# Performance work log

Measured on AMD Instinct MI355X. Metric: run time of the kernel, lower is better.

## Reference

```python
import jax, jax.numpy as jnp
import numpy as np

N = 50000      # nodes
E = 800000     # edges
H = 4          # attention heads
C = 64         # per-head channels (channel_in = channel_out = 64)
DIN = 128      # raw node feature dim (lazy Linear infers this)
D1 = H * C     # 256 = channel_in*4 concat dim
EPS = 1e-16    # PyG softmax eps
LN_EPS = 1e-5


def setup_inputs() -> dict:
    key = jax.random.key(0)
    ks = jax.random.split(key, 20)
    p = lambda k, shape: jax.random.normal(k, shape, jnp.float32) * 0.05
    return {
        "x": jax.random.normal(ks[0], (N, DIN), jnp.float32),
        "edge_index": jax.random.randint(ks[1], (2, E), 0, N, jnp.int32),
        # conv1 (GATConv with separate src/dst transforms, bipartite lazy mode)
        "Wsrc1": p(ks[2], (DIN, D1)), "Wdst1": p(ks[3], (DIN, D1)),
        "atts1": p(ks[4], (H, C)), "attd1": p(ks[5], (H, C)), "b1": p(ks[6], (D1,)),
        # lin1 skip
        "Wlin1": p(ks[7], (DIN, D1)), "blin1": p(ks[8], (D1,)),
        # LayerNorm
        "gamma": jnp.ones((D1,), jnp.float32), "beta": jnp.zeros((D1,), jnp.float32),
        # conv2
        "Wsrc2": p(ks[9], (D1, D1)), "Wdst2": p(ks[10], (D1, D1)),
        "atts2": p(ks[11], (H, C)), "attd2": p(ks[12], (H, C)), "b2": p(ks[13], (D1,)),
        # lin2 skip
        "Wlin2": p(ks[14], (D1, D1)), "blin2": p(ks[15], (D1,)),
    }


def gat_conv(x, src, dst, Wsrc, Wdst, atts, attd, bias):
    """PyG GATConv: gather -> leaky_relu score -> segment softmax over dst -> scatter-add."""
    n = x.shape[0]
    xs = (x @ Wsrc).reshape(n, H, C)   # source-side transform
    xd = (x @ Wdst).reshape(n, H, C)   # destination-side transform
    a_s = jnp.sum(xs * atts, axis=-1)  # [N,H]
    a_d = jnp.sum(xd * attd, axis=-1)  # [N,H]
    e = jax.nn.leaky_relu(a_s[src] + a_d[dst], 0.2)          # [E,H]
    m = jax.ops.segment_max(e, dst, num_segments=n)           # [N,H]
    m = jnp.where(jnp.isfinite(m), m, 0.0)                    # nodes with no in-edges
    ex = jnp.exp(e - m[dst])
    den = jax.ops.segment_sum(ex, dst, num_segments=n)
    alpha = ex / (den[dst] + EPS)                             # [E,H]
    out = jax.ops.segment_sum(xs[src] * alpha[:, :, None], dst, num_segments=n)
    return out.reshape(n, H * C) + bias                       # concat heads + bias


def reference(x, edge_index, Wsrc1, Wdst1, atts1, attd1, b1, Wlin1, blin1,
              gamma, beta, Wsrc2, Wdst2, atts2, attd2, b2, Wlin2, blin2):
    src, dst = edge_index[0], edge_index[1]
    h = gat_conv(x, src, dst, Wsrc1, Wdst1, atts1, attd1, b1) + x @ Wlin1 + blin1
    mu = jnp.mean(h, axis=-1, keepdims=True)
    var = jnp.mean((h - mu) ** 2, axis=-1, keepdims=True)
    h = (h - mu) * jax.lax.rsqrt(var + LN_EPS) * gamma + beta
    h = jax.nn.relu(h)
    out = gat_conv(h, src, dst, Wsrc2, Wdst2, atts2, attd2, b2) + h @ Wlin2 + blin2
    return out
```

## Files before the change

kernel.cpp:

```cpp
#include <hip/hip_runtime.h>
#include <float.h>

constexpr int DIN = 128;
constexpr int D1  = 256;
constexpr int HH  = 4;
constexpr int CC  = 64;

typedef _Float16 f16;
typedef __attribute__((ext_vector_type(2))) _Float16 f16x2;
typedef __attribute__((ext_vector_type(4))) _Float16 f16x4;
typedef __attribute__((ext_vector_type(8))) _Float16 f16x8;
typedef __attribute__((ext_vector_type(4))) float f32x4;

#if __has_builtin(__builtin_amdgcn_fdot2)
#define HAS_FDOT2 1
#else
#define HAS_FDOT2 0
#endif

__device__ __forceinline__ float wave_sum(float v) {
    #pragma unroll
    for (int off = 32; off > 0; off >>= 1) v += __shfl_down(v, off, 64);
    return v;
}

__global__ __launch_bounds__(256) void pack_w_all_kernel(
        const float* __restrict__ Wsrc1, const float* __restrict__ Wlin1,
        const float* __restrict__ Wsrc2, const float* __restrict__ Wlin2,
        f16* __restrict__ WpS1, f16* __restrict__ WpL1,
        f16* __restrict__ WpS2, f16* __restrict__ WpL2) {
    int idx = blockIdx.x * 256 + threadIdx.x;
    const float *Wa, *Wb;
    f16 *Wpa, *Wpb;
    if (idx < DIN * D1) { Wa = Wsrc1; Wb = Wlin1; Wpa = WpS1; Wpb = WpL1; }
    else {
        idx -= DIN * D1;
        if (idx >= D1 * D1) return;
        Wa = Wsrc2; Wb = Wlin2; Wpa = WpS2; Wpb = WpL2;
    }
    int j    = idx & 7;
    int lane = (idx >> 3) & 63;
    int t    = idx >> 9;
    int ct   = t & 15, kt = t >> 4;
    int k    = kt * 32 + (lane >> 4) * 8 + j;
    int col  = ct * 16 + (lane & 15);
    size_t widx = (size_t)k * D1 + col;
    Wpa[idx] = (f16)Wa[widx];
    Wpb[idx] = (f16)Wb[widx];
}

__global__ __launch_bounds__(512) void make_v_all_kernel(
        const float* __restrict__ Wsrc1, const float* __restrict__ Wdst1,
        const float* __restrict__ atts1, const float* __restrict__ attd1,
        const float* __restrict__ Wsrc2, const float* __restrict__ Wdst2,
        const float* __restrict__ atts2, const float* __restrict__ attd2,
        float* __restrict__ Vs1, float* __restrict__ Vd1,
        float* __restrict__ Vs2, float* __restrict__ Vd2) {
    int kb = blockIdx.x;
    int w = threadIdx.x >> 6, lane = threadIdx.x & 63;
    int mat = w >> 2, h = w & 3;
    const float *W, *att;
    float* V;
    int k;
    if (kb < DIN) {
        k = kb;
        W = mat ? Wdst1 : Wsrc1; att = mat ? attd1 : atts1; V = mat ? Vd1 : Vs1;
    } else {
        k = kb - DIN;
        W = mat ? Wdst2 : Wsrc2; att = mat ? attd2 : atts2; V = mat ? Vd2 : Vs2;
    }
    float v = W[(size_t)k * D1 + h * CC + lane] * att[h * CC + lane];
    v = wave_sum(v);
    if (lane == 0) V[k * HH + h] = v;
}

__global__ __launch_bounds__(256) void cvt_scores_kernel(
        const float* __restrict__ X, const float* __restrict__ Vs,
        const float* __restrict__ Vd, f16* __restrict__ X16,
        float* __restrict__ a_s, float* __restrict__ a_d, int n) {
    constexpr int K = DIN, C = 32, SH = 5;
    __shared__ float4 VsL[K + 4];
    __shared__ float4 VdL[K + 4];
    for (int k = threadIdx.x; k < K; k += 256) {
        int ki = k + (k >> SH);
        VsL[ki] = reinterpret_cast<const float4*>(Vs)[k];
        VdL[ki] = reinterpret_cast<const float4*>(Vd)[k];
    }
    __syncthreads();

    const int lane  = threadIdx.x & 63;
    const int wid   = threadIdx.x >> 6;
    const int node  = blockIdx.x * 64 + wid * 16 + (lane >> 2);
    const int chunk = lane & 3;
    const int nodec = min(node, n - 1);
    const float* xp = X + (size_t)nodec * K + chunk * C;

    float xv[C];
    #pragma unroll
    for (int b = 0; b < C / 4; ++b) {
        float4 v = reinterpret_cast<const float4*>(xp)[b];
        xv[b * 4 + 0] = v.x; xv[b * 4 + 1] = v.y;
        xv[b * 4 + 2] = v.z; xv[b * 4 + 3] = v.w;
    }
    if (node < n) {
        f16* op = X16 + (size_t)node * K + chunk * C;
        #pragma unroll
        for (int b = 0; b < C / 8; ++b) {
            f16x8 o;
            #pragma unroll
            for (int t = 0; t < 8; ++t) o[t] = (f16)xv[b * 8 + t];
            reinterpret_cast<f16x8*>(op)[b] = o;
        }
    }

    float ps0 = 0.f, ps1 = 0.f, ps2 = 0.f, ps3 = 0.f;
    float pd0 = 0.f, pd1 = 0.f, pd2 = 0.f, pd3 = 0.f;
    #pragma unroll
    for (int t = 0; t < C; ++t) {
        int k  = chunk * C + t;
        int ki = k + (k >> SH);
        float xf = xv[t];
        float4 vs = VsL[ki];
        float4 vd = VdL[ki];
        ps0 = fmaf(xf, vs.x, ps0); ps1 = fmaf(xf, vs.y, ps1);
        ps2 = fmaf(xf, vs.z, ps2); ps3 = fmaf(xf, vs.w, ps3);
        pd0 = fmaf(xf, vd.x, pd0); pd1 = fmaf(xf, vd.y, pd1);
        pd2 = fmaf(xf, vd.z, pd2); pd3 = fmaf(xf, vd.w, pd3);
    }
    #pragma unroll
    for (int off = 1; off <= 2; off <<= 1) {
        ps0 += __shfl_xor(ps0, off, 64); ps1 += __shfl_xor(ps1, off, 64);
        ps2 += __shfl_xor(ps2, off, 64); ps3 += __shfl_xor(ps3, off, 64);
        pd0 += __shfl_xor(pd0, off, 64); pd1 += __shfl_xor(pd1, off, 64);
        pd2 += __shfl_xor(pd2, off, 64); pd3 += __shfl_xor(pd3, off, 64);
    }
    if (node < n) {
        float psv = chunk == 0 ? ps0 : chunk == 1 ? ps1 : chunk == 2 ? ps2 : ps3;
        float pdv = chunk == 0 ? pd0 : chunk == 1 ? pd1 : chunk == 2 ? pd2 : pd3;
        a_s[node * 4 + chunk] = psv;
        a_d[node * 4 + chunk] = pdv;
    }
}

__global__ __launch_bounds__(256) void deg_kernel(
        const int* __restrict__ dst, int* __restrict__ deg, int ne) {
    int e = blockIdx.x * 256 + threadIdx.x;
    if (e < ne) atomicAdd(deg + dst[e], 1);
}

__global__ __launch_bounds__(1024) void scan_phase1(
        const int* __restrict__ deg, int* __restrict__ partial,
        int* __restrict__ blocksum, int n) {
    __shared__ int tmp[1024];
    const int tid = threadIdx.x;
    int i = blockIdx.x * 1024 + tid;
    int v = (i < n) ? deg[i] : 0;
    tmp[tid] = v;
    __syncthreads();
    #pragma unroll
    for (int off = 1; off < 1024; off <<= 1) {
        int t = (tid >= off) ? tmp[tid - off] : 0;
        __syncthreads();
        tmp[tid] += t;
        __syncthreads();
    }
    if (i < n) partial[i] = tmp[tid];
    if (tid == 1023) blocksum[blockIdx.x] = tmp[1023];
}

__global__ __launch_bounds__(64) void scan_phase2(int* __restrict__ bs, int nb) {
    int lane = threadIdx.x;
    if (nb <= 64) {
        int v = (lane < nb) ? bs[lane] : 0;
        #pragma unroll
        for (int off = 1; off < 64; off <<= 1) {
            int t = __shfl_up(v, off, 64);
            if (lane >= off) v += t;
        }
        if (lane < nb) bs[lane] = v;
    } else if (lane == 0) {
        int acc = 0;
        for (int i = 0; i < nb; ++i) { acc += bs[i]; bs[i] = acc; }
    }
}

__global__ __launch_bounds__(1024) void scan_phase3(
        const int* __restrict__ partial, const int* __restrict__ bs,
        const int* __restrict__ deg, int* __restrict__ rowptr,
        int* __restrict__ degcur, int n) {
    int i = blockIdx.x * 1024 + threadIdx.x;
    if (i >= n) return;
    int add  = blockIdx.x ? bs[blockIdx.x - 1] : 0;
    int incl = partial[i] + add;
    rowptr[i + 1] = incl;
    degcur[i] = incl - deg[i];
    if (i == 0) rowptr[0] = 0;
}

__global__ __launch_bounds__(256) void fill_kernel(
        const int* __restrict__ src, const int* __restrict__ dst,
        int* __restrict__ cursor, int* __restrict__ srcs_csr, int ne) {
    int e = blockIdx.x * 256 + threadIdx.x;
    if (e >= ne) return;
    int pos = atomicAdd(cursor + dst[e], 1);
    srcs_csr[pos] = src[e];
}

template <int K, typename TO2>
__global__ __launch_bounds__(256) void gemm_dual_mfma(
        const f16* __restrict__ A, const f16* __restrict__ Wp1,
        const f16* __restrict__ Wp2, const float* __restrict__ bias1,
        const float* __restrict__ bias2, f16* __restrict__ O1,
        TO2* __restrict__ O2, int n) {
    constexpr int KT = K / 32;
    const int lane = threadIdx.x & 63;
    const int w    = threadIdx.x >> 6;
    const int row0 = blockIdx.x * 64;
    const int col0 = w * 64;

    f32x4 acc1[4][4], acc2[4][4];
    const f32x4 zero = {0.f, 0.f, 0.f, 0.f};
    #pragma unroll
    for (int i = 0; i < 4; ++i)
        #pragma unroll
        for (int j = 0; j < 4; ++j) { acc1[i][j] = zero; acc2[i][j] = zero; }

    const f16* Arow[4];
    #pragma unroll
    for (int rf = 0; rf < 4; ++rf) {
        int ar = min(row0 + rf * 16 + (lane & 15), n - 1);
        Arow[rf] = A + (size_t)ar * K + (lane >> 4) * 8;
    }
    const f16* Wb1 = Wp1 + ((size_t)(w * 4) * 64 + lane) * 8;
    const f16* Wb2 = Wp2 + ((size_t)(w * 4) * 64 + lane) * 8;

    #pragma unroll
    for (int kt = 0; kt < KT; ++kt) {
        f16x8 a[4];
        #pragma unroll
        for (int rf = 0; rf < 4; ++rf)
            a[rf] = *reinterpret_cast<const f16x8*>(Arow[rf] + kt * 32);
        #pragma unroll
        for (int cf = 0; cf < 4; ++cf) {
            f16x8 b1v = *reinterpret_cast<const f16x8*>(Wb1 + (size_t)(kt * 16 + cf) * 512);
            f16x8 b2v = *reinterpret_cast<const f16x8*>(Wb2 + (size_t)(kt * 16 + cf) * 512);
            #pragma unroll
            for (int rf = 0; rf < 4; ++rf) {
                acc1[rf][cf] = __builtin_amdgcn_mfma_f32_16x16x32_f16(a[rf], b1v, acc1[rf][cf], 0, 0, 0);
                acc2[rf][cf] = __builtin_amdgcn_mfma_f32_16x16x32_f16(a[rf], b2v, acc2[rf][cf], 0, 0, 0);
            }
        }
    }

    #pragma unroll
    for (int cf = 0; cf < 4; ++cf) {
        const int col = col0 + cf * 16 + (lane & 15);
        const float bsum = bias1[col] + bias2[col];
        #pragma unroll
        for (int rf = 0; rf < 4; ++rf) {
            #pragma unroll
            for (int r = 0; r < 4; ++r) {
                const int row = row0 + rf * 16 + (lane >> 4) * 4 + r;
                if (row < n) {
                    O1[(size_t)row * D1 + col] = (f16)acc1[rf][cf][r];
                    O2[(size_t)row * D1 + col] = (TO2)(acc2[rf][cf][r] + bsum);
                }
            }
        }
    }
}

__device__ __forceinline__ float sel4(float4 v, int h) {
    return h == 0 ? v.x : h == 1 ? v.y : h == 2 ? v.z : v.w;
}
__device__ __forceinline__ float4 lrelu4(float4 as, float4 ad) {
    float4 e;
    e.x = as.x + ad.x; e.x = e.x > 0.f ? e.x : 0.2f * e.x;
    e.y = as.y + ad.y; e.y = e.y > 0.f ? e.y : 0.2f * e.y;
    e.z = as.z + ad.z; e.z = e.z > 0.f ? e.z : 0.2f * e.z;
    e.w = as.w + ad.w; e.w = e.w > 0.f ? e.w : 0.2f * e.w;
    return e;
}

#define ALDS_STRIDE 66

__device__ __forceinline__ float4 gat_node_acc(
        const int* __restrict__ srcs, const float* __restrict__ a_s,
        const f16* __restrict__ xs, f16* __restrict__ alds,
        float4 ad4, int base, int deg, int lane) {
    const int h = lane >> 4;
    float4 den = {0.f, 0.f, 0.f, 0.f};
    float4 acc = {0.f, 0.f, 0.f, 0.f};
    const f16* arow = alds + h * ALDS_STRIDE;

    for (int c0 = 0; c0 < deg; c0 += 64) {
        const int cnt = min(64, deg - c0);
        const int idx = c0 + lane;
        const bool valid = idx < deg;
        const int sl = srcs[base + min(idx, deg - 1)];
        {
            float4 as = *reinterpret_cast<const float4*>(a_s + (size_t)sl * 4);
            float4 e = lrelu4(as, ad4);
            float a0 = valid ? __expf(e.x) : 0.f;
            float a1 = valid ? __expf(e.y) : 0.f;
            float a2 = valid ? __expf(e.z) : 0.f;
            float a3 = valid ? __expf(e.w) : 0.f;
            den.x += a0; den.y += a1; den.z += a2; den.w += a3;
            alds[0 * ALDS_STRIDE + lane] = (f16)a0;
            alds[1 * ALDS_STRIDE + lane] = (f16)a1;
            alds[2 * ALDS_STRIDE + lane] = (f16)a2;
            alds[3 * ALDS_STRIDE + lane] = (f16)a3;
        }
        asm volatile("s_waitcnt lgkmcnt(0)" ::: "memory");

        const int sv = sl;
        for (int i = 0; i < cnt; i += 4) {
            int s1 = __shfl(sv, i, 64);
            int s2 = __shfl(sv, i + 1, 64);
            int s3 = __shfl(sv, i + 2, 64);
            int s4 = __shfl(sv, i + 3, 64);
            f16x2 alA = *reinterpret_cast<const f16x2*>(arow + i);
            f16x2 alB = *reinterpret_cast<const f16x2*>(arow + i + 2);
            uint2 x1 = *reinterpret_cast<const uint2*>(xs + (size_t)s1 * D1 + lane * 4);
            uint2 x2 = *reinterpret_cast<const uint2*>(xs + (size_t)s2 * D1 + lane * 4);
            uint2 x3 = *reinterpret_cast<const uint2*>(xs + (size_t)s3 * D1 + lane * 4);
            uint2 x4 = *reinterpret_cast<const uint2*>(xs + (size_t)s4 * D1 + lane * 4);
#if HAS_FDOT2
            unsigned pA0 = __builtin_amdgcn_perm(x1.x, x2.x, 0x01000504u);
            unsigned pA1 = __builtin_amdgcn_perm(x1.x, x2.x, 0x03020706u);
            unsigned pA2 = __builtin_amdgcn_perm(x1.y, x2.y, 0x01000504u);
            unsigned pA3 = __builtin_amdgcn_perm(x1.y, x2.y, 0x03020706u);
            acc.x = __builtin_amdgcn_fdot2(__builtin_bit_cast(f16x2, pA0), alA, acc.x, false);
            acc.y = __builtin_amdgcn_fdot2(__builtin_bit_cast(f16x2, pA1), alA, acc.y, false);
            acc.z = __builtin_amdgcn_fdot2(__builtin_bit_cast(f16x2, pA2), alA, acc.z, false);
            acc.w = __builtin_amdgcn_fdot2(__builtin_bit_cast(f16x2, pA3), alA, acc.w, false);
            unsigned pB0 = __builtin_amdgcn_perm(x3.x, x4.x, 0x01000504u);
            unsigned pB1 = __builtin_amdgcn_perm(x3.x, x4.x, 0x03020706u);
            unsigned pB2 = __builtin_amdgcn_perm(x3.y, x4.y, 0x01000504u);
            unsigned pB3 = __builtin_amdgcn_perm(x3.y, x4.y, 0x03020706u);
            acc.x = __builtin_amdgcn_fdot2(__builtin_bit_cast(f16x2, pB0), alB, acc.x, false);
            acc.y = __builtin_amdgcn_fdot2(__builtin_bit_cast(f16x2, pB1), alB, acc.y, false);
            acc.z = __builtin_amdgcn_fdot2(__builtin_bit_cast(f16x2, pB2), alB, acc.z, false);
            acc.w = __builtin_amdgcn_fdot2(__builtin_bit_cast(f16x2, pB3), alB, acc.w, false);
#else
            f16x4 a1v = __builtin_bit_cast(f16x4, x1);
            f16x4 a2v = __builtin_bit_cast(f16x4, x2);
            f16x4 a3v = __builtin_bit_cast(f16x4, x3);
            f16x4 a4v = __builtin_bit_cast(f16x4, x4);
            float w1 = (float)alA.x, w2 = (float)alA.y;
            float w3 = (float)alB.x, w4 = (float)alB.y;
            acc.x = fmaf((float)a1v[0], w1, acc.x); acc.x = fmaf((float)a2v[0], w2, acc.x);
            acc.y = fmaf((float)a1v[1], w1, acc.y); acc.y = fmaf((float)a2v[1], w2, acc.y);
            acc.z = fmaf((float)a1v[2], w1, acc.z); acc.z = fmaf((float)a2v[2], w2, acc.z);
            acc.w = fmaf((float)a1v[3], w1, acc.w); acc.w = fmaf((float)a4v[3], w2, acc.w);
            acc.x = fmaf((float)a3v[0], w3, acc.x); acc.x = fmaf((float)a4v[0], w4, acc.x);
            acc.y = fmaf((float)a3v[1], w3, acc.y); acc.y = fmaf((float)a4v[1], w4, acc.y);
            acc.z = fmaf((float)a3v[2], w3, acc.z); acc.z = fmaf((float)a4v[2], w4, acc.z);
            acc.w = fmaf((float)a3v[3], w3, acc.w); acc.w = fmaf((float)a4v[3], w4, acc.w);
#endif
        }
    }

    #pragma unroll
    for (int off = 1; off < 64; off <<= 1) {
        den.x += __shfl_xor(den.x, off, 64);
        den.y += __shfl_xor(den.y, off, 64);
        den.z += __shfl_xor(den.z, off, 64);
        den.w += __shfl_xor(den.w, off, 64);
    }
    const float invd = 1.f / (sel4(den, h) + 1e-16f);
    acc.x *= invd; acc.y *= invd; acc.z *= invd; acc.w *= invd;
    return acc;
}

__global__ __launch_bounds__(256) void gat_gather_ln_kernel(
        const int* __restrict__ rowptr, const int* __restrict__ srcs,
        const float* __restrict__ a_s1, const float* __restrict__ a_d1,
        const f16* __restrict__ xs, const f16* __restrict__ skip,
        const float* __restrict__ gamma, const float* __restrict__ beta,
        const float* __restrict__ Vs2, const float* __restrict__ Vd2,
        f16* __restrict__ hout, float* __restrict__ a_s2,
        float* __restrict__ a_d2, int n) {
    __shared__ f16 alpha_lds[4][4 * ALDS_STRIDE];
    const int wid = threadIdx.x >> 6, lane = threadIdx.x & 63;
    const int d = blockIdx.x * 4 + wid;
    if (d >= n) return;
    const int base = rowptr[d];
    const int deg  = rowptr[d + 1] - base;

    float4 acc = {0.f, 0.f, 0.f, 0.f};
    if (deg > 0) {
        const float4 ad4 = *reinterpret_cast<const float4*>(a_d1 + (size_t)d * 4);
        acc = gat_node_acc(srcs, a_s1, xs, alpha_lds[wid], ad4, base, deg, lane);
    }

    f16x4 sk = *reinterpret_cast<const f16x4*>(skip + (size_t)d * D1 + lane * 4);
    float4 v;
    v.x = acc.x + (float)sk[0];
    v.y = acc.y + (float)sk[1];
    v.z = acc.z + (float)sk[2];
    v.w = acc.w + (float)sk[3];

    float s  = v.x + v.y + v.z + v.w;
    float sq = v.x * v.x + v.y * v.y + v.z * v.z + v.w * v.w;
    #pragma unroll
    for (int off = 32; off > 0; off >>= 1) {
        s  += __shfl_down(s, off, 64);
        sq += __shfl_down(sq, off, 64);
    }
    s  = __shfl(s, 0, 64);
    sq = __shfl(sq, 0, 64);
    float mu  = s * (1.f / 256.f);
    float var = sq * (1.f / 256.f) - mu * mu;
    float rstd = rsqrtf(var + 1e-5f);
    float4 g = *reinterpret_cast<const float4*>(gamma + lane * 4);
    float4 b = *reinterpret_cast<const float4*>(beta + lane * 4);
    f16x4 o;
    o[0] = (f16)fmaxf((v.x - mu) * rstd * g.x + b.x, 0.f);
    o[1] = (f16)fmaxf((v.y - mu) * rstd * g.y + b.y, 0.f);
    o[2] = (f16)fmaxf((v.z - mu) * rstd * g.z + b.z, 0.f);
    o[3] = (f16)fmaxf((v.w - mu) * rstd * g.w + b.w, 0.f);
    *reinterpret_cast<f16x4*>(hout + (size_t)d * D1 + lane * 4) = o;

    float of0 = (float)o[0], of1 = (float)o[1], of2 = (float)o[2], of3 = (float)o[3];
    const float4* V4s = reinterpret_cast<const float4*>(Vs2);
    const float4* V4d = reinterpret_cast<const float4*>(Vd2);
    float4 r0 = V4s[lane * 4 + 0], r1 = V4s[lane * 4 + 1];
    float4 r2 = V4s[lane * 4 + 2], r3 = V4s[lane * 4 + 3];
    float4 ps;
    ps.x = of0 * r0.x + of1 * r1.x + of2 * r2.x + of3 * r3.x;
    ps.y = of0 * r0.y + of1 * r1.y + of2 * r2.y + of3 * r3.y;
    ps.z = of0 * r0.z + of1 * r1.z + of2 * r2.z + of3 * r3.z;
    ps.w = of0 * r0.w + of1 * r1.w + of2 * r2.w + of3 * r3.w;
    r0 = V4d[lane * 4 + 0]; r1 = V4d[lane * 4 + 1];
    r2 = V4d[lane * 4 + 2]; r3 = V4d[lane * 4 + 3];
    float4 pd;
    pd.x = of0 * r0.x + of1 * r1.x + of2 * r2.x + of3 * r3.x;
    pd.y = of0 * r0.y + of1 * r1.y + of2 * r2.y + of3 * r3.y;
    pd.z = of0 * r0.z + of1 * r1.z + of2 * r2.z + of3 * r3.z;
    pd.w = of0 * r0.w + of1 * r1.w + of2 * r2.w + of3 * r3.w;
    #pragma unroll
    for (int off = 1; off < 64; off <<= 1) {
        ps.x += __shfl_xor(ps.x, off, 64); ps.y += __shfl_xor(ps.y, off, 64);
        ps.z += __shfl_xor(ps.z, off, 64); ps.w += __shfl_xor(ps.w, off, 64);
        pd.x += __shfl_xor(pd.x, off, 64); pd.y += __shfl_xor(pd.y, off, 64);
        pd.z += __shfl_xor(pd.z, off, 64); pd.w += __shfl_xor(pd.w, off, 64);
    }
    if (lane == 0) {
        *reinterpret_cast<float4*>(a_s2 + (size_t)d * 4) = ps;
        *reinterpret_cast<float4*>(a_d2 + (size_t)d * 4) = pd;
    }
}

__global__ __launch_bounds__(256) void gat_gather_out_kernel(
        const int* __restrict__ rowptr, const int* __restrict__ srcs,
        const float* __restrict__ a_s, const float* __restrict__ a_d,
        const f16* __restrict__ xs, float* __restrict__ out, int n) {
    __shared__ f16 alpha_lds[4][4 * ALDS_STRIDE];
    const int wid = threadIdx.x >> 6, lane = threadIdx.x & 63;
    const int d = blockIdx.x * 4 + wid;
    if (d >= n) return;
    const int base = rowptr[d];
    const int deg  = rowptr[d + 1] - base;
    if (deg == 0) return;
    const float4 ad4 = *reinterpret_cast<const float4*>(a_d + (size_t)d * 4);
    float4 acc = gat_node_acc(srcs, a_s, xs, alpha_lds[wid], ad4, base, deg, lane);
    float* o = out + (size_t)d * D1 + lane * 4;
    float4 ov = *reinterpret_cast<const float4*>(o);
    ov.x += acc.x; ov.y += acc.y; ov.z += acc.z; ov.w += acc.w;
    *reinterpret_cast<float4*>(o) = ov;
}

extern "C" void kernel_launch(void* const* d_in, const int* in_sizes, int n_in,
                              void* d_out, int out_size, void* d_ws, size_t ws_size,
                              hipStream_t stream) {
    const float* x     = (const float*)d_in[0];
    const int*   ei    = (const int*)d_in[1];
    const float* Wsrc1 = (const float*)d_in[2];
    const float* Wdst1 = (const float*)d_in[3];
    const float* atts1 = (const float*)d_in[4];
    const float* attd1 = (const float*)d_in[5];
    const float* b1    = (const float*)d_in[6];
    const float* Wlin1 = (const float*)d_in[7];
    const float* blin1 = (const float*)d_in[8];
    const float* gamma = (const float*)d_in[9];
    const float* beta  = (const float*)d_in[10];
    const float* Wsrc2 = (const float*)d_in[11];
    const float* Wdst2 = (const float*)d_in[12];
    const float* atts2 = (const float*)d_in[13];
    const float* attd2 = (const float*)d_in[14];
    const float* b2    = (const float*)d_in[15];
    const float* Wlin2 = (const float*)d_in[16];
    const float* blin2 = (const float*)d_in[17];

    const int n  = in_sizes[0] / DIN;
    const int ne = in_sizes[1] / 2;
    const int* src = ei;
    const int* dst = ei + ne;

    char* w8 = (char*)d_ws;
    size_t off = 0;
    auto alloc = [&](size_t bytes) -> void* {
        void* p = w8 + off;
        off += (bytes + 255) & ~(size_t)255;
        return p;
    };
    f16*  h16    = (f16*)alloc((size_t)n * D1 * 2);
    f16*  x16    = h16;
    f16*  xs16   = (f16*)alloc((size_t)n * D1 * 2);
    f16*  skip1  = (f16*)alloc((size_t)n * D1 * 2);
    float* a_s1  = (float*)alloc((size_t)n * HH * 4);
    float* a_d1  = (float*)alloc((size_t)n * HH * 4);
    float* a_s2  = (float*)alloc((size_t)n * HH * 4);
    float* a_d2  = (float*)alloc((size_t)n * HH * 4);
    float* Vs1   = (float*)alloc((size_t)D1 * HH * 4);
    float* Vd1   = (float*)alloc((size_t)D1 * HH * 4);
    float* Vs2   = (float*)alloc((size_t)D1 * HH * 4);
    float* Vd2   = (float*)alloc((size_t)D1 * HH * 4);
    int* rowptr   = (int*)alloc(((size_t)n + 1) * 4);
    int* degbuf   = (int*)alloc((size_t)n * 4);
    int* degcur   = (int*)alloc((size_t)n * 4);
    int* partial  = (int*)alloc((size_t)n * 4);
    int* blocksum = (int*)alloc(1024 * 4);
    int* srcs_csr = (int*)alloc((size_t)ne * 4);
    f16* WpS1  = (f16*)alloc((size_t)DIN * D1 * 2);
    f16* WpL1  = (f16*)alloc((size_t)DIN * D1 * 2);
    f16* WpS2  = (f16*)alloc((size_t)D1 * D1 * 2);
    f16* WpL2  = (f16*)alloc((size_t)D1 * D1 * 2);

    float* out = (float*)d_out;

    const int nb_node4  = (n + 3) / 4;
    const int nb_node64 = (n + 63) / 64;
    const int nb_e      = (ne + 255) / 256;
    const int nb_gemm   = (n + 63) / 64;
    const int nb_scan   = (n + 1023) / 1024;
    const int nb_pack   = (DIN * D1 + D1 * D1 + 255) / 256;

    hipMemsetAsync(degbuf, 0, (size_t)n * 4, stream);
    deg_kernel<<<nb_e, 256, 0, stream>>>(dst, degbuf, ne);
    scan_phase1<<<nb_scan, 1024, 0, stream>>>(degbuf, partial, blocksum, n);
    scan_phase2<<<1, 64, 0, stream>>>(blocksum, nb_scan);
    scan_phase3<<<nb_scan, 1024, 0, stream>>>(partial, blocksum, degbuf, rowptr, degcur, n);
    fill_kernel<<<nb_e, 256, 0, stream>>>(src, dst, degcur, srcs_csr, ne);
    pack_w_all_kernel<<<nb_pack, 256, 0, stream>>>(Wsrc1, Wlin1, Wsrc2, Wlin2,
                                                   WpS1, WpL1, WpS2, WpL2);
    make_v_all_kernel<<<DIN + D1, 512, 0, stream>>>(Wsrc1, Wdst1, atts1, attd1,
                                                    Wsrc2, Wdst2, atts2, attd2,
                                                    Vs1, Vd1, Vs2, Vd2);

    cvt_scores_kernel<<<nb_node64, 256, 0, stream>>>(x, Vs1, Vd1, x16, a_s1, a_d1, n);
    gemm_dual_mfma<DIN, f16><<<nb_gemm, 256, 0, stream>>>(x16, WpS1, WpL1, b1, blin1, xs16, skip1, n);
    gat_gather_ln_kernel<<<nb_node4, 256, 0, stream>>>(rowptr, srcs_csr, a_s1, a_d1, xs16,
                                                       skip1, gamma, beta, Vs2, Vd2,
                                                       h16, a_s2, a_d2, n);

    gemm_dual_mfma<D1, float><<<nb_gemm, 256, 0, stream>>>(h16, WpS2, WpL2, b2, blin2, xs16, out, n);
    gat_gather_out_kernel<<<nb_node4, 256, 0, stream>>>(rowptr, srcs_csr, a_s2, a_d2, xs16, out, n);
}
```

Measured before the change: 330.0 us.

## Split GAT aggregation into alpha precompute and column-sliced gather kernels

Attention coefficients are now computed and normalized once per edge into a head-major f16 buffer by a separate kernel. The aggregation is then split across 8 column slices per node, with 8 lanes per node. Blocks with the same slice index touch the same narrow column band of xs, which is meant to improve cache locality of the random gathers. LayerNorm and the second-layer skip add become separate passes over an intermediate buffer. The cost is extra launches and extra global traffic for the alpha and gather buffers, plus f16 rounding of the normalized alphas.

```diff
diff --git a/kernel.cpp b/kernel.cpp
--- a/kernel.cpp
+++ b/kernel.cpp
@@ -206,12 +206,12 @@
     srcs_csr[pos] = src[e];
 }
 
-template <int K, typename TO2>
+template <int K>
 __global__ __launch_bounds__(256) void gemm_dual_mfma(
         const f16* __restrict__ A, const f16* __restrict__ Wp1,
         const f16* __restrict__ Wp2, const float* __restrict__ bias1,
         const float* __restrict__ bias2, f16* __restrict__ O1,
-        TO2* __restrict__ O2, int n) {
+        f16* __restrict__ O2, int n) {
     constexpr int KT = K / 32;
     const int lane = threadIdx.x & 63;
     const int w    = threadIdx.x >> 6;
@@ -263,16 +263,13 @@
                 const int row = row0 + rf * 16 + (lane >> 4) * 4 + r;
                 if (row < n) {
                     O1[(size_t)row * D1 + col] = (f16)acc1[rf][cf][r];
-                    O2[(size_t)row * D1 + col] = (TO2)(acc2[rf][cf][r] + bsum);
+                    O2[(size_t)row * D1 + col] = (f16)(acc2[rf][cf][r] + bsum);
                 }
             }
         }
     }
 }
 
-__device__ __forceinline__ float sel4(float4 v, int h) {
-    return h == 0 ? v.x : h == 1 ? v.y : h == 2 ? v.z : v.w;
-}
 __device__ __forceinline__ float4 lrelu4(float4 as, float4 ad) {
     float4 e;
     e.x = as.x + ad.x; e.x = e.x > 0.f ? e.x : 0.2f * e.x;
@@ -282,23 +279,49 @@
     return e;
 }
 
-#define ALDS_STRIDE 66
-
-__device__ __forceinline__ float4 gat_node_acc(
-        const int* __restrict__ srcs, const float* __restrict__ a_s,
-        const f16* __restrict__ xs, f16* __restrict__ alds,
-        float4 ad4, int base, int deg, int lane) {
-    const int h = lane >> 4;
-    float4 den = {0.f, 0.f, 0.f, 0.f};
-    float4 acc = {0.f, 0.f, 0.f, 0.f};
-    const f16* arow = alds + h * ALDS_STRIDE;
-
-    for (int c0 = 0; c0 < deg; c0 += 64) {
-        const int cnt = min(64, deg - c0);
-        const int idx = c0 + lane;
-        const bool valid = idx < deg;
-        const int sl = srcs[base + min(idx, deg - 1)];
-        {
+__global__ __launch_bounds__(256) void alpha16_kernel(
+        const int* __restrict__ rowptr, const int* __restrict__ srcs,
+        const float* __restrict__ a_s, const float* __restrict__ a_d,
+        f16* __restrict__ alphaT, int ne, int n) {
+    const int lane = threadIdx.x & 63;
+    const int wid  = threadIdx.x >> 6;
+    const int g    = lane & 15;
+    const int d    = blockIdx.x * 16 + wid * 4 + (lane >> 4);
+    if (d >= n) return;
+    const int base = rowptr[d];
+    const int deg  = rowptr[d + 1] - base;
+    if (deg == 0) return;
+    const float4 ad4 = *reinterpret_cast<const float4*>(a_d + (size_t)d * 4);
+
+    if (deg <= 16) {
+        const bool valid = g < deg;
+        const int sl = srcs[base + min(g, deg - 1)];
+        float4 as = *reinterpret_cast<const float4*>(a_s + (size_t)sl * 4);
+        float4 e = lrelu4(as, ad4);
+        float a0 = valid ? __expf(e.x) : 0.f;
+        float a1 = valid ? __expf(e.y) : 0.f;
+        float a2 = valid ? __expf(e.z) : 0.f;
+        float a3 = valid ? __expf(e.w) : 0.f;
+        float4 den = {a0, a1, a2, a3};
+        #pragma unroll
+        for (int off = 1; off < 16; off <<= 1) {
+            den.x += __shfl_xor(den.x, off, 16);
+            den.y += __shfl_xor(den.y, off, 16);
+            den.z += __shfl_xor(den.z, off, 16);
+            den.w += __shfl_xor(den.w, off, 16);
+        }
+        if (valid) {
+            alphaT[0 * (size_t)ne + base + g] = (f16)(a0 / (den.x + 1e-16f));
+            alphaT[1 * (size_t)ne + base + g] = (f16)(a1 / (den.y + 1e-16f));
+            alphaT[2 * (size_t)ne + base + g] = (f16)(a2 / (den.z + 1e-16f));
+            alphaT[3 * (size_t)ne + base + g] = (f16)(a3 / (den.w + 1e-16f));
+        }
+    } else {
+        float4 den = {0.f, 0.f, 0.f, 0.f};
+        for (int c0 = 0; c0 < deg; c0 += 16) {
+            int idx = c0 + g;
+            bool valid = idx < deg;
+            int sl = srcs[base + min(idx, deg - 1)];
             float4 as = *reinterpret_cast<const float4*>(a_s + (size_t)sl * 4);
             float4 e = lrelu4(as, ad4);
             float a0 = valid ? __expf(e.x) : 0.f;
@@ -306,100 +329,142 @@
             float a2 = valid ? __expf(e.z) : 0.f;
             float a3 = valid ? __expf(e.w) : 0.f;
             den.x += a0; den.y += a1; den.z += a2; den.w += a3;
-            alds[0 * ALDS_STRIDE + lane] = (f16)a0;
-            alds[1 * ALDS_STRIDE + lane] = (f16)a1;
-            alds[2 * ALDS_STRIDE + lane] = (f16)a2;
-            alds[3 * ALDS_STRIDE + lane] = (f16)a3;
-        }
-        asm volatile("s_waitcnt lgkmcnt(0)" ::: "memory");
-
-        const int sv = sl;
-        for (int i = 0; i < cnt; i += 4) {
-            int s1 = __shfl(sv, i, 64);
-            int s2 = __shfl(sv, i + 1, 64);
-            int s3 = __shfl(sv, i + 2, 64);
-            int s4 = __shfl(sv, i + 3, 64);
-            f16x2 alA = *reinterpret_cast<const f16x2*>(arow + i);
-            f16x2 alB = *reinterpret_cast<const f16x2*>(arow + i + 2);
-            uint2 x1 = *reinterpret_cast<const uint2*>(xs + (size_t)s1 * D1 + lane * 4);
-            uint2 x2 = *reinterpret_cast<const uint2*>(xs + (size_t)s2 * D1 + lane * 4);
-            uint2 x3 = *reinterpret_cast<const uint2*>(xs + (size_t)s3 * D1 + lane * 4);
-            uint2 x4 = *reinterpret_cast<const uint2*>(xs + (size_t)s4 * D1 + lane * 4);
+            if (valid) {
+                alphaT[0 * (size_t)ne + base + idx] = (f16)a0;
+                alphaT[1 * (size_t)ne + base + idx] = (f16)a1;
+                alphaT[2 * (size_t)ne + base + idx] = (f16)a2;
+                alphaT[3 * (size_t)ne + base + idx] = (f16)a3;
+            }
+        }
+        #pragma unroll
+        for (int off = 1; off < 16; off <<= 1) {
+            den.x += __shfl_xor(den.x, off, 16);
+            den.y += __shfl_xor(den.y, off, 16);
+            den.z += __shfl_xor(den.z, off, 16);
+            den.w += __shfl_xor(den.w, off, 16);
+        }
+        float i0 = 1.f / (den.x + 1e-16f);
+        float i1 = 1.f / (den.y + 1e-16f);
+        float i2 = 1.f / (den.z + 1e-16f);
+        float i3 = 1.f / (den.w + 1e-16f);
+        for (int idx = g; idx < deg; idx += 16) {
+            alphaT[0 * (size_t)ne + base + idx] = (f16)((float)alphaT[0 * (size_t)ne + base + idx] * i0);
+            alphaT[1 * (size_t)ne + base + idx] = (f16)((float)alphaT[1 * (size_t)ne + base + idx] * i1);
+            alphaT[2 * (size_t)ne + base + idx] = (f16)((float)alphaT[2 * (size_t)ne + base + idx] * i2);
+            alphaT[3 * (size_t)ne + base + idx] = (f16)((float)alphaT[3 * (size_t)ne + base + idx] * i3);
+        }
+    }
+}
+
+__device__ __forceinline__ float4 gather_slice_acc(
+        const int* __restrict__ srcs, const f16* __restrict__ ap,
+        const f16* __restrict__ xs, int base, int deg, int coloff, int g) {
+    float4 acc = {0.f, 0.f, 0.f, 0.f};
+    for (int c0 = 0; c0 < deg; c0 += 8) {
+        const int idx = c0 + g;
+        const int sl = __builtin_nontemporal_load(srcs + base + min(idx, deg - 1));
+        int abit = 0;
+        if (idx < deg)
+            abit = (int)__builtin_nontemporal_load(
+                reinterpret_cast<const unsigned short*>(ap + base + idx));
+        const int cnt = min(8, deg - c0);
+        for (int i = 0; i < cnt; i += 2) {
+            int s1 = __shfl(sl, i, 8);
+            int s2 = __shfl(sl, i + 1, 8);
+            int a1 = __shfl(abit, i, 8);
+            int a2 = __shfl(abit, i + 1, 8);
+            unsigned au = (unsigned)(a1 & 0xffff) | ((unsigned)a2 << 16);
+            f16x2 al2 = __builtin_bit_cast(f16x2, au);
+            uint2 x1 = *reinterpret_cast<const uint2*>(xs + (size_t)s1 * D1 + coloff);
+            uint2 x2 = *reinterpret_cast<const uint2*>(xs + (size_t)s2 * D1 + coloff);
 #if HAS_FDOT2
-            unsigned pA0 = __builtin_amdgcn_perm(x1.x, x2.x, 0x01000504u);
-            unsigned pA1 = __builtin_amdgcn_perm(x1.x, x2.x, 0x03020706u);
-            unsigned pA2 = __builtin_amdgcn_perm(x1.y, x2.y, 0x01000504u);
-            unsigned pA3 = __builtin_amdgcn_perm(x1.y, x2.y, 0x03020706u);
-            acc.x = __builtin_amdgcn_fdot2(__builtin_bit_cast(f16x2, pA0), alA, acc.x, false);
-            acc.y = __builtin_amdgcn_fdot2(__builtin_bit_cast(f16x2, pA1), alA, acc.y, false);
-            acc.z = __builtin_amdgcn_fdot2(__builtin_bit_cast(f16x2, pA2), alA, acc.z, false);
-            acc.w = __builtin_amdgcn_fdot2(__builtin_bit_cast(f16x2, pA3), alA, acc.w, false);
-            unsigned pB0 = __builtin_amdgcn_perm(x3.x, x4.x, 0x01000504u);
-            unsigned pB1 = __builtin_amdgcn_perm(x3.x, x4.x, 0x03020706u);
-            unsigned pB2 = __builtin_amdgcn_perm(x3.y, x4.y, 0x01000504u);
-            unsigned pB3 = __builtin_amdgcn_perm(x3.y, x4.y, 0x03020706u);
-            acc.x = __builtin_amdgcn_fdot2(__builtin_bit_cast(f16x2, pB0), alB, acc.x, false);
-            acc.y = __builtin_amdgcn_fdot2(__builtin_bit_cast(f16x2, pB1), alB, acc.y, false);
-            acc.z = __builtin_amdgcn_fdot2(__builtin_bit_cast(f16x2, pB2), alB, acc.z, false);
-            acc.w = __builtin_amdgcn_fdot2(__builtin_bit_cast(f16x2, pB3), alB, acc.w, false);
+            unsigned p0 = __builtin_amdgcn_perm(x1.x, x2.x, 0x01000504u);
+            unsigned p1 = __builtin_amdgcn_perm(x1.x, x2.x, 0x03020706u);
+            unsigned p2 = __builtin_amdgcn_perm(x1.y, x2.y, 0x01000504u);
+            unsigned p3 = __builtin_amdgcn_perm(x1.y, x2.y, 0x03020706u);
+            acc.x = __builtin_amdgcn_fdot2(__builtin_bit_cast(f16x2, p0), al2, acc.x, false);
+            acc.y = __builtin_amdgcn_fdot2(__builtin_bit_cast(f16x2, p1), al2, acc.y, false);
+            acc.z = __builtin_amdgcn_fdot2(__builtin_bit_cast(f16x2, p2), al2, acc.z, false);
+            acc.w = __builtin_amdgcn_fdot2(__builtin_bit_cast(f16x2, p3), al2, acc.w, false);
 #else
             f16x4 a1v = __builtin_bit_cast(f16x4, x1);
             f16x4 a2v = __builtin_bit_cast(f16x4, x2);
-            f16x4 a3v = __builtin_bit_cast(f16x4, x3);
-            f16x4 a4v = __builtin_bit_cast(f16x4, x4);
-            float w1 = (float)alA.x, w2 = (float)alA.y;
-            float w3 = (float)alB.x, w4 = (float)alB.y;
+            float w1 = (float)al2.x, w2 = (float)al2.y;
             acc.x = fmaf((float)a1v[0], w1, acc.x); acc.x = fmaf((float)a2v[0], w2, acc.x);
             acc.y = fmaf((float)a1v[1], w1, acc.y); acc.y = fmaf((float)a2v[1], w2, acc.y);
             acc.z = fmaf((float)a1v[2], w1, acc.z); acc.z = fmaf((float)a2v[2], w2, acc.z);
-            acc.w = fmaf((float)a1v[3], w1, acc.w); acc.w = fmaf((float)a4v[3], w2, acc.w);
-            acc.x = fmaf((float)a3v[0], w3, acc.x); acc.x = fmaf((float)a4v[0], w4, acc.x);
-            acc.y = fmaf((float)a3v[1], w3, acc.y); acc.y = fmaf((float)a4v[1], w4, acc.y);
-            acc.z = fmaf((float)a3v[2], w3, acc.z); acc.z = fmaf((float)a4v[2], w4, acc.z);
-            acc.w = fmaf((float)a3v[3], w3, acc.w); acc.w = fmaf((float)a4v[3], w4, acc.w);
+            acc.w = fmaf((float)a1v[3], w1, acc.w); acc.w = fmaf((float)a2v[3], w2, acc.w);
 #endif
         }
     }
-
-    #pragma unroll
-    for (int off = 1; off < 64; off <<= 1) {
-        den.x += __shfl_xor(den.x, off, 64);
-        den.y += __shfl_xor(den.y, off, 64);
-        den.z += __shfl_xor(den.z, off, 64);
-        den.w += __shfl_xor(den.w, off, 64);
-    }
-    const float invd = 1.f / (sel4(den, h) + 1e-16f);
-    acc.x *= invd; acc.y *= invd; acc.z *= invd; acc.w *= invd;
     return acc;
 }
 
-__global__ __launch_bounds__(256) void gat_gather_ln_kernel(
+__global__ __launch_bounds__(256) void gather_cs_kernel(
         const int* __restrict__ rowptr, const int* __restrict__ srcs,
-        const float* __restrict__ a_s1, const float* __restrict__ a_d1,
-        const f16* __restrict__ xs, const f16* __restrict__ skip,
+        const f16* __restrict__ alphaT, const f16* __restrict__ xs,
+        f16* __restrict__ gbuf, int ne, int n) {
+    const int s    = blockIdx.x & 7;
+    const int nb   = blockIdx.x >> 3;
+    const int lane = threadIdx.x & 63;
+    const int wid  = threadIdx.x >> 6;
+    const int g    = lane & 7;
+    const int node = nb * 32 + wid * 8 + (lane >> 3);
+    if (node >= n) return;
+    const int base = rowptr[node];
+    const int deg  = rowptr[node + 1] - base;
+    const int coloff = s * 32 + g * 4;
+    float4 acc = gather_slice_acc(srcs, alphaT + (size_t)(s >> 1) * ne, xs,
+                                  base, deg, coloff, g);
+    f16x4 o = {(f16)acc.x, (f16)acc.y, (f16)acc.z, (f16)acc.w};
+    __builtin_nontemporal_store(o,
+        reinterpret_cast<f16x4*>(gbuf + (size_t)node * D1 + coloff));
+}
+
+__global__ __launch_bounds__(256) void gather_cs_out_kernel(
+        const int* __restrict__ rowptr, const int* __restrict__ srcs,
+        const f16* __restrict__ alphaT, const f16* __restrict__ xs,
+        const f16* __restrict__ skip2, float* __restrict__ out, int ne, int n) {
+    const int s    = blockIdx.x & 7;
+    const int nb   = blockIdx.x >> 3;
+    const int lane = threadIdx.x & 63;
+    const int wid  = threadIdx.x >> 6;
+    const int g    = lane & 7;
+    const int node = nb * 32 + wid * 8 + (lane >> 3);
+    if (node >= n) return;
+    const int base = rowptr[node];
+    const int deg  = rowptr[node + 1] - base;
+    const int coloff = s * 32 + g * 4;
+    float4 acc = gather_slice_acc(srcs, alphaT + (size_t)(s >> 1) * ne, xs,
+                                  base, deg, coloff, g);
+    f16x4 sk = __builtin_nontemporal_load(
+        reinterpret_cast<const f16x4*>(skip2 + (size_t)node * D1 + coloff));
+    f32x4 ov;
+    ov[0] = acc.x + (float)sk[0];
+    ov[1] = acc.y + (float)sk[1];
+    ov[2] = acc.z + (float)sk[2];
+    ov[3] = acc.w + (float)sk[3];
+    __builtin_nontemporal_store(ov,
+        reinterpret_cast<f32x4*>(out + (size_t)node * D1 + coloff));
+}
+
+__global__ __launch_bounds__(256) void ln_scores_kernel(
+        const f16* __restrict__ gbuf, const f16* __restrict__ skip,
         const float* __restrict__ gamma, const float* __restrict__ beta,
         const float* __restrict__ Vs2, const float* __restrict__ Vd2,
         f16* __restrict__ hout, float* __restrict__ a_s2,
         float* __restrict__ a_d2, int n) {
-    __shared__ f16 alpha_lds[4][4 * ALDS_STRIDE];
     const int wid = threadIdx.x >> 6, lane = threadIdx.x & 63;
     const int d = blockIdx.x * 4 + wid;
     if (d >= n) return;
-    const int base = rowptr[d];
-    const int deg  = rowptr[d + 1] - base;
-
-    float4 acc = {0.f, 0.f, 0.f, 0.f};
-    if (deg > 0) {
-        const float4 ad4 = *reinterpret_cast<const float4*>(a_d1 + (size_t)d * 4);
-        acc = gat_node_acc(srcs, a_s1, xs, alpha_lds[wid], ad4, base, deg, lane);
-    }
-
+
+    f16x4 gv = *reinterpret_cast<const f16x4*>(gbuf + (size_t)d * D1 + lane * 4);
     f16x4 sk = *reinterpret_cast<const f16x4*>(skip + (size_t)d * D1 + lane * 4);
     float4 v;
-    v.x = acc.x + (float)sk[0];
-    v.y = acc.y + (float)sk[1];
-    v.z = acc.z + (float)sk[2];
-    v.w = acc.w + (float)sk[3];
+    v.x = (float)gv[0] + (float)sk[0];
+    v.y = (float)gv[1] + (float)sk[1];
+    v.z = (float)gv[2] + (float)sk[2];
+    v.w = (float)gv[3] + (float)sk[3];
 
     float s  = v.x + v.y + v.z + v.w;
     float sq = v.x * v.x + v.y * v.y + v.z * v.z + v.w * v.w;
@@ -450,25 +515,6 @@
         *reinterpret_cast<float4*>(a_s2 + (size_t)d * 4) = ps;
         *reinterpret_cast<float4*>(a_d2 + (size_t)d * 4) = pd;
     }
-}
-
-__global__ __launch_bounds__(256) void gat_gather_out_kernel(
-        const int* __restrict__ rowptr, const int* __restrict__ srcs,
-        const float* __restrict__ a_s, const float* __restrict__ a_d,
-        const f16* __restrict__ xs, float* __restrict__ out, int n) {
-    __shared__ f16 alpha_lds[4][4 * ALDS_STRIDE];
-    const int wid = threadIdx.x >> 6, lane = threadIdx.x & 63;
-    const int d = blockIdx.x * 4 + wid;
-    if (d >= n) return;
-    const int base = rowptr[d];
-    const int deg  = rowptr[d + 1] - base;
-    if (deg == 0) return;
-    const float4 ad4 = *reinterpret_cast<const float4*>(a_d + (size_t)d * 4);
-    float4 acc = gat_node_acc(srcs, a_s, xs, alpha_lds[wid], ad4, base, deg, lane);
-    float* o = out + (size_t)d * D1 + lane * 4;
-    float4 ov = *reinterpret_cast<const float4*>(o);
-    ov.x += acc.x; ov.y += acc.y; ov.z += acc.z; ov.w += acc.w;
-    *reinterpret_cast<float4*>(o) = ov;
 }
 
 extern "C" void kernel_launch(void* const* d_in, const int* in_sizes, int n_in,
@@ -509,6 +555,7 @@
     f16*  x16    = h16;
     f16*  xs16   = (f16*)alloc((size_t)n * D1 * 2);
     f16*  skip1  = (f16*)alloc((size_t)n * D1 * 2);
+    f16*  gbuf   = (f16*)alloc((size_t)n * D1 * 2);
     float* a_s1  = (float*)alloc((size_t)n * HH * 4);
     float* a_d1  = (float*)alloc((size_t)n * HH * 4);
     float* a_s2  = (float*)alloc((size_t)n * HH * 4);
@@ -523,6 +570,7 @@
     int* partial  = (int*)alloc((size_t)n * 4);
     int* blocksum = (int*)alloc(1024 * 4);
     int* srcs_csr = (int*)alloc((size_t)ne * 4);
+    f16* alphaT   = (f16*)alloc((size_t)ne * HH * 2);
     f16* WpS1  = (f16*)alloc((size_t)DIN * D1 * 2);
     f16* WpL1  = (f16*)alloc((size_t)DIN * D1 * 2);
     f16* WpS2  = (f16*)alloc((size_t)D1 * D1 * 2);
@@ -531,13 +579,15 @@
     float* out = (float*)d_out;
 
     const int nb_node4  = (n + 3) / 4;
+    const int nb_node16 = (n + 15) / 16;
     const int nb_node64 = (n + 63) / 64;
     const int nb_e      = (ne + 255) / 256;
     const int nb_gemm   = (n + 63) / 64;
     const int nb_scan   = (n + 1023) / 1024;
     const int nb_pack   = (DIN * D1 + D1 * D1 + 255) / 256;
-
-    hipMemsetAsync(degbuf, 0, (size_t)n * 4, stream);
+    const int nb_gcs    = 8 * ((n + 31) / 32);
+
+    (void)hipMemsetAsync(degbuf, 0, (size_t)n * 4, stream);
     deg_kernel<<<nb_e, 256, 0, stream>>>(dst, degbuf, ne);
     scan_phase1<<<nb_scan, 1024, 0, stream>>>(degbuf, partial, blocksum, n);
     scan_phase2<<<1, 64, 0, stream>>>(blocksum, nb_scan);
@@ -550,11 +600,14 @@
                                                     Vs1, Vd1, Vs2, Vd2);
 
     cvt_scores_kernel<<<nb_node64, 256, 0, stream>>>(x, Vs1, Vd1, x16, a_s1, a_d1, n);
-    gemm_dual_mfma<DIN, f16><<<nb_gemm, 256, 0, stream>>>(x16, WpS1, WpL1, b1, blin1, xs16, skip1, n);
-    gat_gather_ln_kernel<<<nb_node4, 256, 0, stream>>>(rowptr, srcs_csr, a_s1, a_d1, xs16,
-                                                       skip1, gamma, beta, Vs2, Vd2,
-                                                       h16, a_s2, a_d2, n);
-
-    gemm_dual_mfma<D1, float><<<nb_gemm, 256, 0, stream>>>(h16, WpS2, WpL2, b2, blin2, xs16, out, n);
-    gat_gather_out_kernel<<<nb_node4, 256, 0, stream>>>(rowptr, srcs_csr, a_s2, a_d2, xs16, out, n);
-}
+    alpha16_kernel<<<nb_node16, 256, 0, stream>>>(rowptr, srcs_csr, a_s1, a_d1, alphaT, ne, n);
+    gemm_dual_mfma<DIN><<<nb_gemm, 256, 0, stream>>>(x16, WpS1, WpL1, b1, blin1, xs16, skip1, n);
+    gather_cs_kernel<<<nb_gcs, 256, 0, stream>>>(rowptr, srcs_csr, alphaT, xs16, gbuf, ne, n);
+    ln_scores_kernel<<<nb_node4, 256, 0, stream>>>(gbuf, skip1, gamma, beta, Vs2, Vd2,
+                                                   h16, a_s2, a_d2, n);
+
+    alpha16_kernel<<<nb_node16, 256, 0, stream>>>(rowptr, srcs_csr, a_s2, a_d2, alphaT, ne, n);
+    gemm_dual_mfma<D1><<<nb_gemm, 256, 0, stream>>>(h16, WpS2, WpL2, b2, blin2, xs16, skip1, n);
+    gather_cs_out_kernel<<<nb_gcs, 256, 0, stream>>>(rowptr, srcs_csr, alphaT, xs16,
+                                                     skip1, out, ne, n);
+}
```

Result: slower. 456.9 us (+38.5%).
